# Performance work log

Hardware: AMD Instinct MI355X
Metric: run time of the kernel (lower is better)

Reference implementation:

```python
import jax, jax.numpy as jnp
import numpy as np

D_MODEL = 1024
D_STATE = 16
D_CONV = 4
EXPAND = 2
D_INNER = EXPAND * D_MODEL          # 2048
DT_RANK = D_MODEL // 16             # 64
BATCH, SEQ = 4, 2048


def setup_inputs() -> dict:
    key = jax.random.key(0)
    ks = jax.random.split(key, 8)
    s = lambda k, shape, sc=0.02: jax.random.normal(k, shape, jnp.float32) * sc
    x = jax.random.normal(ks[0], (BATCH, SEQ, D_MODEL), jnp.float32)
    tau = jax.random.uniform(ks[1], (BATCH, SEQ), jnp.float32) * 7200.0  # seconds
    # S4D-real init for A
    A_log = jnp.log(jnp.broadcast_to(jnp.arange(1, D_STATE + 1, dtype=jnp.float32), (D_INNER, D_STATE)))
    return dict(
        x=x, tau=tau,
        ln_g=jnp.ones((D_MODEL,), jnp.float32),
        ln_b=jnp.zeros((D_MODEL,), jnp.float32),
        in_proj_w=s(ks[2], (2 * D_INNER, D_MODEL)),
        conv_w=s(ks[3], (D_INNER, 1, D_CONV), 0.1),   # depthwise [O, I/g=1, K]
        conv_b=jnp.zeros((D_INNER,), jnp.float32),
        x_proj_w=s(ks[4], (DT_RANK + 2 * D_STATE, D_INNER)),
        dt_proj_w=s(ks[5], (D_INNER, DT_RANK), 0.1),
        dt_proj_b=jnp.full((D_INNER,), -4.6, jnp.float32),  # softplus ~ 0.01
        A_log=A_log,
        D=jnp.ones((D_INNER,), jnp.float32),
        out_proj_w=s(ks[6], (D_MODEL, D_INNER)),
        log_decay=jnp.full((D_MODEL,), -3.0, jnp.float32),
    )


def _mamba_block(x, tau, ln_g, ln_b, in_proj_w, conv_w, conv_b, x_proj_w,
                 dt_proj_w, dt_proj_b, A_log, D, out_proj_w, log_decay):
    # LayerNorm(d_model)
    mu = jnp.mean(x, axis=-1, keepdims=True)
    var = jnp.var(x, axis=-1, keepdims=True)
    xn = (x - mu) * jax.lax.rsqrt(var + 1e-5) * ln_g + ln_b

    # in_proj -> split into conv branch and gate branch, each [B, L, d_inner]
    xz = jnp.einsum('bld,ed->ble', xn, in_proj_w)
    x_in, z = jnp.split(xz, 2, axis=-1)

    # causal depthwise conv1d over time
    xc = jax.lax.conv_general_dilated(
        x_in.transpose(0, 2, 1), conv_w, (1,), [(D_CONV - 1, 0)],
        dimension_numbers=('NCH', 'OIH', 'NCH'), feature_group_count=D_INNER)
    u = jax.nn.silu(xc.transpose(0, 2, 1) + conv_b)          # [B, L, d_inner]

    # input-dependent SSM params
    x_dbl = jnp.einsum('ble,fe->blf', u, x_proj_w)
    dt, Bm, Cm = jnp.split(x_dbl, [DT_RANK, DT_RANK + D_STATE], axis=-1)
    delta = jax.nn.softplus(jnp.einsum('blr,dr->bld', dt, dt_proj_w) + dt_proj_b)
    A = -jnp.exp(A_log)                                       # [d_inner, d_state]

    # selective scan: h_t = exp(dt*A)*h + dt*u*B_t ; y_t = <h_t, C_t>
    def step(h, inp):
        d_t, B_t, C_t, u_t = inp                              # [B,d],[B,n],[B,n],[B,d]
        h = jnp.exp(d_t[..., None] * A) * h + (d_t * u_t)[..., None] * B_t[:, None, :]
        return h, jnp.einsum('bdn,bn->bd', h, C_t)

    h0 = jnp.zeros((x.shape[0], D_INNER, D_STATE), x.dtype)
    xs = (delta.transpose(1, 0, 2), Bm.transpose(1, 0, 2),
          Cm.transpose(1, 0, 2), u.transpose(1, 0, 2))
    _, ys = jax.lax.scan(step, h0, xs)
    y = ys.transpose(1, 0, 2) + u * D
    y = y * jax.nn.silu(z)
    h_out = jnp.einsum('ble,de->bld', y, out_proj_w)          # mamba output [B,L,d_model]

    # ZOH time-decay gate + residual (dropout = identity in eval)
    tau_h = jnp.maximum(tau / 3600.0, 1e-4)[..., None]
    gate = jnp.exp(-jax.nn.softplus(log_decay) * tau_h)
    return x + h_out * gate


def reference(x, tau, ln_g, ln_b, in_proj_w, conv_w, conv_b, x_proj_w,
              dt_proj_w, dt_proj_b, A_log, D, out_proj_w, log_decay):
    return _mamba_block(x, tau, ln_g, ln_b, in_proj_w, conv_w, conv_b, x_proj_w,
                        dt_proj_w, dt_proj_b, A_log, D, out_proj_w, log_decay)
```

## Files before the change

kernel.cpp:

```cpp
#include <hip/hip_runtime.h>

typedef unsigned short u16;
typedef unsigned int u32;
typedef short s16x8 __attribute__((ext_vector_type(8)));
typedef u16 u16x8 __attribute__((ext_vector_type(8)));
typedef float f32x4 __attribute__((ext_vector_type(4)));

#define TOK 8192
#define DM 1024
#define DI 2048
#define DS 16
#define DR 64
#define NCHUNK 64
#define CH 32
#define XPN 96
#define XP_SPLIT 4
#define CONV_T 16

#define SBAR() do { asm volatile("" ::: "memory"); __builtin_amdgcn_s_barrier(); asm volatile("" ::: "memory"); } while (0)
#define WAITVM(N) do { asm volatile("s_waitcnt vmcnt(" #N ")" ::: "memory"); __builtin_amdgcn_sched_barrier(0); } while (0)
#define WAITLGKM0() do { asm volatile("s_waitcnt lgkmcnt(0)" ::: "memory"); __builtin_amdgcn_sched_barrier(0); } while (0)

__device__ __forceinline__ u16 f2bf(float f) {
    u32 u = __float_as_uint(f);
    u32 r = (u + 0x7fffu + ((u >> 16) & 1u)) >> 16;
    return (u16)r;
}
__device__ __forceinline__ float bf2f(u16 h) {
    return __uint_as_float(((u32)h) << 16);
}
__device__ __forceinline__ float softplus_f(float x) {
    return (x > 15.f) ? x : __logf(1.f + __expf(x));
}
__device__ __forceinline__ void unpack8(const uint4 v, float* o) {
    o[0] = __uint_as_float(v.x << 16); o[1] = __uint_as_float(v.x & 0xffff0000u);
    o[2] = __uint_as_float(v.y << 16); o[3] = __uint_as_float(v.y & 0xffff0000u);
    o[4] = __uint_as_float(v.z << 16); o[5] = __uint_as_float(v.z & 0xffff0000u);
    o[6] = __uint_as_float(v.w << 16); o[7] = __uint_as_float(v.w & 0xffff0000u);
}
__device__ __forceinline__ void async16(u16* lds, const u16* g) {
    __builtin_amdgcn_global_load_lds(
        (const __attribute__((address_space(1))) void*)g,
        (__attribute__((address_space(3))) void*)lds, 16, 0, 0);
}

__global__ __launch_bounds__(256) void cvt_all(
    const float* __restrict__ in_w, const float* __restrict__ xp_w,
    const float* __restrict__ dt_w, const float* __restrict__ out_w,
    const float* __restrict__ tau, const float* __restrict__ log_decay,
    u16* __restrict__ wi, u16* __restrict__ wxp, u16* __restrict__ wdt,
    u16* __restrict__ wout, float* __restrict__ th, float* __restrict__ sd) {
    const int b = blockIdx.x;
    const float* src; u16* dst; int i;
    if (b < 4096)      { src = in_w;  dst = wi;   i = b * 256 + threadIdx.x; }
    else if (b < 4288) { src = xp_w;  dst = wxp;  i = (b - 4096) * 256 + threadIdx.x; }
    else if (b < 4416) { src = dt_w;  dst = wdt;  i = (b - 4288) * 256 + threadIdx.x; }
    else if (b < 6464) { src = out_w; dst = wout; i = (b - 4416) * 256 + threadIdx.x; }
    else {
        int j = (b - 6464) * 256 + threadIdx.x;
        if (j < TOK) th[j] = fmaxf(tau[j] * (1.f / 3600.f), 1e-4f);
        if (j < DM)  sd[j] = softplus_f(log_decay[j]);
        return;
    }
    float4 v = ((const float4*)src)[i];
    ushort4 o;
    o.x = f2bf(v.x); o.y = f2bf(v.y); o.z = f2bf(v.z); o.w = f2bf(v.w);
    ((ushort4*)dst)[i] = o;
}

__global__ __launch_bounds__(256) void ln_kernel(const float* __restrict__ x,
                                                 const float* __restrict__ g,
                                                 const float* __restrict__ bb,
                                                 u16* __restrict__ xn) {
    const int tok = blockIdx.x;
    const float4 v = ((const float4*)(x + (size_t)tok * DM))[threadIdx.x];
    float s = v.x + v.y + v.z + v.w;
    float sq = v.x * v.x + v.y * v.y + v.z * v.z + v.w * v.w;
#pragma unroll
    for (int off = 32; off; off >>= 1) {
        s += __shfl_xor(s, off);
        sq += __shfl_xor(sq, off);
    }
    __shared__ float red[8];
    const int wv = threadIdx.x >> 6;
    if ((threadIdx.x & 63) == 0) { red[wv] = s; red[4 + wv] = sq; }
    __syncthreads();
    s = red[0] + red[1] + red[2] + red[3];
    sq = red[4] + red[5] + red[6] + red[7];
    const float mean = s * (1.f / DM);
    const float var = sq * (1.f / DM) - mean * mean;
    const float rstd = rsqrtf(var + 1e-5f);
    const float4 gv = ((const float4*)g)[threadIdx.x];
    const float4 bv = ((const float4*)bb)[threadIdx.x];
    ushort4 o;
    o.x = f2bf((v.x - mean) * rstd * gv.x + bv.x);
    o.y = f2bf((v.y - mean) * rstd * gv.y + bv.y);
    o.z = f2bf((v.z - mean) * rstd * gv.z + bv.z);
    o.w = f2bf((v.w - mean) * rstd * gv.w + bv.w);
    ((ushort4*)(xn + (size_t)tok * DM))[threadIdx.x] = o;
}

template <int EPI>
__global__ __launch_bounds__(256, 2) void gemm128(
    const u16* __restrict__ A, int lda,
    const u16* __restrict__ W, int ldw, int K,
    u16* __restrict__ Cxi, u16* __restrict__ Cz,
    float* __restrict__ Cf,
    const float* __restrict__ xres, const float* __restrict__ th,
    const float* __restrict__ sd) {
    __shared__ __align__(16) u16 lds[2 * 16384];
    const int tid = threadIdx.x;
    const int wave = tid >> 6, lane = tid & 63;
    const int wm = wave >> 1, wn = wave & 1;
    const int fl = lane & 15, fh = lane >> 4;
    int bm, bn;
    if (EPI == 0) {
        const int swz = ((int)blockIdx.x & 7) * 256 + ((int)blockIdx.x >> 3);
        const int rg = swz >> 5, wi_ = swz & 31;
        bm = (rg >> 2) * 4 + (wi_ >> 3);
        bn = (rg & 3) * 8 + (wi_ & 7);
    } else {
        const int swz = ((int)blockIdx.x & 7) * 64 + ((int)blockIdx.x >> 3);
        const int rg = swz >> 4, wi_ = swz & 15;
        bm = (rg >> 1) * 4 + (wi_ >> 2);
        bn = (rg & 1) * 4 + (wi_ & 3);
    }
    const int NT = K >> 6;

    const int r0 = tid >> 3;
    const int cb = ((tid & 7) ^ (r0 & 7)) << 3;
    const int rA = bm * 128 + r0;
    const int rB = bn * 128 + r0;

    f32x4 acc[4][4];
#pragma unroll
    for (int m = 0; m < 4; m++)
#pragma unroll
        for (int n = 0; n < 4; n++) acc[m][n] = f32x4{0.f, 0.f, 0.f, 0.f};

    auto stage = [&](int buf, int k0) {
#pragma unroll
        for (int j = 0; j < 4; j++)
            async16(lds + buf * 16384 + j * 2048 + tid * 8,
                    A + (size_t)(rA + j * 32) * lda + k0 + cb);
#pragma unroll
        for (int j = 0; j < 4; j++)
            async16(lds + buf * 16384 + 8192 + j * 2048 + tid * 8,
                    W + (size_t)(rB + j * 32) * ldw + k0 + cb);
    };
    auto rdA = [&](int buf, int mf, int kk) -> s16x8 {
        int r = wm * 64 + mf * 16 + fl;
        int slot = ((kk << 2) | fh) ^ (fl & 7);
        return *(const s16x8*)(lds + buf * 16384 + r * 64 + slot * 8);
    };
    auto rdB = [&](int buf, int nf, int kk) -> s16x8 {
        int r = wn * 64 + nf * 16 + fl;
        int slot = ((kk << 2) | fh) ^ (fl & 7);
        return *(const s16x8*)(lds + buf * 16384 + 8192 + r * 64 + slot * 8);
    };

    stage(0, 0);
    stage(1, 64);
    WAITVM(8);
    SBAR();

    for (int t = 0; t < NT; ++t) {
        const int cur = t & 1;
        s16x8 ah[4][2], bh[4][2];
#pragma unroll
        for (int mf = 0; mf < 4; mf++) { ah[mf][0] = rdA(cur, mf, 0); ah[mf][1] = rdA(cur, mf, 1); }
#pragma unroll
        for (int nf = 0; nf < 4; nf++) { bh[nf][0] = rdB(cur, nf, 0); bh[nf][1] = rdB(cur, nf, 1); }
        WAITLGKM0();
        SBAR();
        if (t + 2 < NT) stage(cur, (t + 2) << 6);
        __builtin_amdgcn_s_setprio(1);
#pragma unroll
        for (int kk = 0; kk < 2; kk++)
#pragma unroll
            for (int mf = 0; mf < 4; mf++)
#pragma unroll
                for (int nf = 0; nf < 4; nf++)
                    acc[mf][nf] = __builtin_amdgcn_mfma_f32_16x16x32_bf16(ah[mf][kk], bh[nf][kk], acc[mf][nf], 0, 0, 0);
        __builtin_amdgcn_s_setprio(0);
        __builtin_amdgcn_sched_barrier(0);
        if (t + 2 < NT) { WAITVM(8); }
        else           { WAITVM(0); }
        SBAR();
    }

#pragma unroll
    for (int mf = 0; mf < 4; mf++)
#pragma unroll
        for (int j = 0; j < 4; j++) {
            int row = bm * 128 + wm * 64 + mf * 16 + fh * 4 + j;
            if (EPI == 0) {
                u16* dst = (bn < 16) ? Cxi : Cz;
                const int cbase = (bn < 16) ? bn * 128 : (bn - 16) * 128;
#pragma unroll
                for (int n = 0; n < 4; n++) {
                    int col = cbase + wn * 64 + n * 16 + fl;
                    dst[(size_t)row * DI + col] = f2bf(acc[mf][n][j]);
                }
            } else {
                float t = th[row];
#pragma unroll
                for (int n = 0; n < 4; n++) {
                    int col = bn * 128 + wn * 64 + n * 16 + fl;
                    size_t idx = (size_t)row * DM + col;
                    Cf[idx] = xres[idx] + acc[mf][n][j] * __expf(-sd[col] * t);
                }
            }
        }
}

__global__ __launch_bounds__(256) void gemm_bt(
    const u16* __restrict__ A, int lda,
    const u16* __restrict__ W,
    u16* __restrict__ Cb, int ldc,
    int M, int N, int K,
    const float* __restrict__ bias) {
    __shared__ u16 As[128 * 32];
    __shared__ u16 Bs[128 * 32];
    const int tid = threadIdx.x;
    const int wave = tid >> 6, lane = tid & 63;
    const int bm = blockIdx.x, bn = blockIdx.y;
    const int srow = lane >> 2, scol = (lane & 3) * 8;
    const int wr = wave >> 1, wc = wave & 1;
    const int fl = lane & 15, fh = lane >> 4;

    f32x4 acc[4][4];
#pragma unroll
    for (int m = 0; m < 4; m++)
#pragma unroll
        for (int n = 0; n < 4; n++) acc[m][n] = f32x4{0.f, 0.f, 0.f, 0.f};

    int ra[2], rb[2];
    u16* ldsA[2]; u16* ldsB[2];
#pragma unroll
    for (int i = 0; i < 2; i++) {
        int r = (wave * 2 + i) * 16 + srow;
        ra[i] = min(bm * 128 + r, M - 1);
        rb[i] = min(bn * 128 + r, N - 1);
        ldsA[i] = As + (wave * 2 + i) * 512 + lane * 8;
        ldsB[i] = Bs + (wave * 2 + i) * 512 + lane * 8;
    }

    for (int k0 = 0; k0 < K; k0 += 32) {
        __syncthreads();
#pragma unroll
        for (int i = 0; i < 2; i++) {
            async16(ldsA[i], A + (size_t)ra[i] * lda + k0 + scol);
            async16(ldsB[i], W + (size_t)rb[i] * K + k0 + scol);
        }
        __syncthreads();
        s16x8 av[4], bv[4];
#pragma unroll
        for (int m = 0; m < 4; m++)
            av[m] = *(const s16x8*)(As + (wr * 64 + m * 16 + fl) * 32 + fh * 8);
#pragma unroll
        for (int n = 0; n < 4; n++)
            bv[n] = *(const s16x8*)(Bs + (wc * 64 + n * 16 + fl) * 32 + fh * 8);
#pragma unroll
        for (int m = 0; m < 4; m++)
#pragma unroll
            for (int n = 0; n < 4; n++)
                acc[m][n] = __builtin_amdgcn_mfma_f32_16x16x32_bf16(av[m], bv[n], acc[m][n], 0, 0, 0);
    }

#pragma unroll
    for (int m = 0; m < 4; m++) {
#pragma unroll
        for (int j = 0; j < 4; j++) {
            int row = bm * 128 + wr * 64 + m * 16 + fh * 4 + j;
            if (row >= M) continue;
#pragma unroll
            for (int n = 0; n < 4; n++) {
                int col = bn * 128 + wc * 64 + n * 16 + fl;
                if (col >= N) continue;
                Cb[(size_t)row * ldc + col] = f2bf(softplus_f(acc[m][n][j] + bias[col]));
            }
        }
    }
}

__global__ __launch_bounds__(256) void xp_gemm(const u16* __restrict__ A,
                                               const u16* __restrict__ W,
                                               float* __restrict__ part) {
    __shared__ u16 As[128 * 64];
    __shared__ u16 Bs[XPN * 64];
    const int tid = threadIdx.x;
    const int wave = tid >> 6, lane = tid & 63;
    const int bm = blockIdx.x, sp = blockIdx.y;
    const int fl = lane & 15, fh = lane >> 4;
    const int trow = tid >> 3, tcol = (tid & 7) * 8;

    f32x4 acc[2][6];
#pragma unroll
    for (int m = 0; m < 2; m++)
#pragma unroll
        for (int n = 0; n < 6; n++) acc[m][n] = f32x4{0.f, 0.f, 0.f, 0.f};

    const int kbeg = sp * (DI / XP_SPLIT);
    for (int k0 = kbeg; k0 < kbeg + DI / XP_SPLIT; k0 += 64) {
        __syncthreads();
#pragma unroll
        for (int i = 0; i < 4; i++)
            async16(As + i * 2048 + tid * 8,
                    A + (size_t)(bm * 128 + i * 32 + trow) * DI + k0 + tcol);
#pragma unroll
        for (int i = 0; i < 3; i++)
            async16(Bs + i * 2048 + tid * 8,
                    W + (size_t)(i * 32 + trow) * DI + k0 + tcol);
        __syncthreads();
#pragma unroll
        for (int kk = 0; kk < 2; kk++) {
            s16x8 av[2], bv[6];
#pragma unroll
            for (int m = 0; m < 2; m++)
                av[m] = *(const s16x8*)(As + (wave * 32 + m * 16 + fl) * 64 + kk * 32 + fh * 8);
#pragma unroll
            for (int n = 0; n < 6; n++)
                bv[n] = *(const s16x8*)(Bs + (n * 16 + fl) * 64 + kk * 32 + fh * 8);
#pragma unroll
            for (int m = 0; m < 2; m++)
#pragma unroll
                for (int n = 0; n < 6; n++)
                    acc[m][n] = __builtin_amdgcn_mfma_f32_16x16x32_bf16(av[m], bv[n], acc[m][n], 0, 0, 0);
        }
    }
    float* dst = part + (size_t)sp * TOK * XPN;
#pragma unroll
    for (int m = 0; m < 2; m++)
#pragma unroll
        for (int j = 0; j < 4; j++) {
            int row = bm * 128 + wave * 32 + m * 16 + fh * 4 + j;
#pragma unroll
            for (int n = 0; n < 6; n++) {
                int col = n * 16 + fl;
                dst[(size_t)row * XPN + col] = acc[m][n][j];
            }
        }
}

__global__ __launch_bounds__(256) void xp_reduce(const float* __restrict__ part,
                                                 u16* __restrict__ out) {
    int i = blockIdx.x * 256 + threadIdx.x;
    if (i >= TOK * XPN) return;
    float s = 0.f;
#pragma unroll
    for (int sp = 0; sp < XP_SPLIT; sp++) s += part[(size_t)sp * TOK * XPN + i];
    out[i] = f2bf(s);
}

__global__ __launch_bounds__(256) void conv_silu_kernel(const u16* __restrict__ xi,
                                                        const float* __restrict__ cw,
                                                        const float* __restrict__ cb,
                                                        u16* __restrict__ u) {
    const int b = blockIdx.y;
    const int l0 = blockIdx.x * CONV_T;
    const int d0 = threadIdx.x * 8;
    float w0[8], w1[8], w2[8], w3[8], bias[8];
#pragma unroll
    for (int e = 0; e < 8; e++) {
        float4 wv = ((const float4*)cw)[d0 + e];
        w0[e] = wv.x; w1[e] = wv.y; w2[e] = wv.z; w3[e] = wv.w;
        bias[e] = cb[d0 + e];
    }
    float win[4][8];
#pragma unroll
    for (int i = 0; i < 3; i++) {
        int l = l0 - 3 + i;
        int slot = (l0 + 1 + i) & 3;
        if (l < 0) {
#pragma unroll
            for (int e = 0; e < 8; e++) win[slot][e] = 0.f;
        } else {
            u16x8 v = *(const u16x8*)(xi + ((size_t)(b * 2048 + l)) * DI + d0);
#pragma unroll
            for (int e = 0; e < 8; e++) win[slot][e] = bf2f(v[e]);
        }
    }
#pragma unroll
    for (int t = 0; t < CONV_T; t++) {
        const int l = l0 + t;
        const size_t tok = (size_t)b * 2048 + l;
        u16x8 v = *(const u16x8*)(xi + tok * DI + d0);
        const int s3 = t & 3;
#pragma unroll
        for (int e = 0; e < 8; e++) win[s3][e] = bf2f(v[e]);
        const int s0 = (t + 1) & 3, s1 = (t + 2) & 3, s2 = (t + 3) & 3;
        u16x8 o;
#pragma unroll
        for (int e = 0; e < 8; e++) {
            float a = bias[e];
            a = fmaf(w0[e], win[s0][e], a);
            a = fmaf(w1[e], win[s1][e], a);
            a = fmaf(w2[e], win[s2][e], a);
            a = fmaf(w3[e], win[s3][e], a);
            o[e] = f2bf(a / (1.f + __expf(-a)));
        }
        *(u16x8*)(u + tok * DI + d0) = o;
    }
}

__global__ __launch_bounds__(256) void scan_passA(const u16* __restrict__ delta,
                                                  const u16* __restrict__ u,
                                                  const u16* __restrict__ xdbl,
                                                  const float* __restrict__ A_log,
                                                  float* __restrict__ qh,
                                                  float* __restrict__ Sarr) {
    const int d = blockIdx.x * 256 + threadIdx.x;
    const int b = blockIdx.y, c = blockIdx.z;
    float Av[16];
#pragma unroll
    for (int n = 0; n < 16; n++) Av[n] = -__expf(A_log[d * 16 + n]);
    bool fast = true;
#pragma unroll
    for (int n = 0; n < 16; n++) fast = fast && (fabsf(Av[n] + (float)(n + 1)) < 1e-4f * (n + 1));
    const bool allfast = __all(fast);

    float h[16];
#pragma unroll
    for (int n = 0; n < 16; n++) h[n] = 0.f;
    float S = 0.f;
    const int l0 = c * CH;
    size_t tok = (size_t)b * 2048 + l0;
    float dt = bf2f(delta[tok * DI + d]);
    float uu = bf2f(u[tok * DI + d]);
    const uint4* bp0 = (const uint4*)(xdbl + tok * 96 + 64);
    uint4 b0 = bp0[0], b1 = bp0[1];
    for (int t = 0; t < CH; ++t) {
        const int tn = (t + 1 < CH) ? t + 1 : t;
        const size_t tokn = (size_t)b * 2048 + l0 + tn;
        float dt_n = bf2f(delta[tokn * DI + d]);
        float uu_n = bf2f(u[tokn * DI + d]);
        const uint4* bpn = (const uint4*)(xdbl + tokn * 96 + 64);
        uint4 b0n = bpn[0], b1n = bpn[1];
        float du = dt * uu;
        float Bv[16];
        unpack8(b0, Bv); unpack8(b1, Bv + 8);
        float e[16];
        if (allfast) {
            float r = __expf(-dt);
            e[0] = r;
#pragma unroll
            for (int n = 1; n < 16; n++) e[n] = e[n - 1] * r;
        } else {
#pragma unroll
            for (int n = 0; n < 16; n++) e[n] = __expf(dt * Av[n]);
        }
#pragma unroll
        for (int n = 0; n < 16; n++) h[n] = fmaf(e[n], h[n], du * Bv[n]);
        S += dt;
        dt = dt_n; uu = uu_n; b0 = b0n; b1 = b1n;
    }
    const size_t base = ((size_t)(c * 4 + b) * 16) * DI + d;
#pragma unroll
    for (int n = 0; n < 16; n++) qh[base + (size_t)n * DI] = h[n];
    Sarr[(size_t)(c * 4 + b) * DI + d] = S;
}

__global__ __launch_bounds__(256) void scan_passB(float* __restrict__ qh,
                                                  const float* __restrict__ Sarr,
                                                  const float* __restrict__ A_log) {
    const int idx = blockIdx.x * 256 + threadIdx.x;
    const int d = idx & (DI - 1);
    const int n = (idx >> 11) & 15;
    const int b = idx >> 15;
    const float Avn = -__expf(A_log[d * 16 + n]);
    float h = 0.f;
    for (int c = 0; c < NCHUNK; c++) {
        const size_t base = ((size_t)(c * 4 + b) * 16 + n) * DI + d;
        const float qv = qh[base];
        const float S = Sarr[(size_t)(c * 4 + b) * DI + d];
        qh[base] = h;
        h = fmaf(__expf(Avn * S), h, qv);
    }
}

__global__ __launch_bounds__(256) void scan_passC(const u16* __restrict__ delta,
                                                  const u16* __restrict__ u,
                                                  const u16* __restrict__ xdbl,
                                                  const u16* __restrict__ z,
                                                  const float* __restrict__ A_log,
                                                  const float* __restrict__ Dvec,
                                                  const float* __restrict__ qh,
                                                  u16* __restrict__ yg) {
    const int d = blockIdx.x * 256 + threadIdx.x;
    const int b = blockIdx.y, c = blockIdx.z;
    float Av[16];
#pragma unroll
    for (int n = 0; n < 16; n++) Av[n] = -__expf(A_log[d * 16 + n]);
    bool fast = true;
#pragma unroll
    for (int n = 0; n < 16; n++) fast = fast && (fabsf(Av[n] + (float)(n + 1)) < 1e-4f * (n + 1));
    const bool allfast = __all(fast);
    const float Dd = Dvec[d];

    float h[16];
    const size_t hbase = ((size_t)(c * 4 + b) * 16) * DI + d;
#pragma unroll
    for (int n = 0; n < 16; n++) h[n] = qh[hbase + (size_t)n * DI];

    const int l0 = c * CH;
    size_t tok = (size_t)b * 2048 + l0;
    float dt = bf2f(delta[tok * DI + d]);
    float uu = bf2f(u[tok * DI + d]);
    float zz = bf2f(z[tok * DI + d]);
    const uint4* bp0 = (const uint4*)(xdbl + tok * 96 + 64);
    uint4 b0 = bp0[0], b1 = bp0[1], c0 = bp0[2], c1 = bp0[3];
    for (int t = 0; t < CH; ++t) {
        const int tn = (t + 1 < CH) ? t + 1 : t;
        const size_t tokn = (size_t)b * 2048 + l0 + tn;
        float dt_n = bf2f(delta[tokn * DI + d]);
        float uu_n = bf2f(u[tokn * DI + d]);
        float zz_n = bf2f(z[tokn * DI + d]);
        const uint4* bpn = (const uint4*)(xdbl + tokn * 96 + 64);
        uint4 b0n = bpn[0], b1n = bpn[1], c0n = bpn[2], c1n = bpn[3];

        float du = dt * uu;
        float Bv[16], Cv[16];
        unpack8(b0, Bv); unpack8(b1, Bv + 8);
        unpack8(c0, Cv); unpack8(c1, Cv + 8);
        float e[16];
        if (allfast) {
            float r = __expf(-dt);
            e[0] = r;
#pragma unroll
            for (int n = 1; n < 16; n++) e[n] = e[n - 1] * r;
        } else {
#pragma unroll
            for (int n = 0; n < 16; n++) e[n] = __expf(dt * Av[n]);
        }
        float y = 0.f;
#pragma unroll
        for (int n = 0; n < 16; n++) {
            h[n] = fmaf(e[n], h[n], du * Bv[n]);
            y = fmaf(h[n], Cv[n], y);
        }
        float sz = zz / (1.f + __expf(-zz));
        const size_t tokc = (size_t)b * 2048 + l0 + t;
        yg[tokc * DI + d] = f2bf((y + uu * Dd) * sz);

        dt = dt_n; uu = uu_n; zz = zz_n;
        b0 = b0n; b1 = b1n; c0 = c0n; c1 = c1n;
    }
}

extern "C" void kernel_launch(void* const* d_in, const int* in_sizes, int n_in,
                              void* d_out, int out_size, void* d_ws, size_t ws_size,
                              hipStream_t stream) {
    const float* x = (const float*)d_in[0];
    const float* tau = (const float*)d_in[1];
    const float* ln_g = (const float*)d_in[2];
    const float* ln_b = (const float*)d_in[3];
    const float* in_proj_w = (const float*)d_in[4];
    const float* conv_w = (const float*)d_in[5];
    const float* conv_b = (const float*)d_in[6];
    const float* x_proj_w = (const float*)d_in[7];
    const float* dt_proj_w = (const float*)d_in[8];
    const float* dt_proj_b = (const float*)d_in[9];
    const float* A_log = (const float*)d_in[10];
    const float* Dvec = (const float*)d_in[11];
    const float* out_proj_w = (const float*)d_in[12];
    const float* log_decay = (const float*)d_in[13];
    float* out = (float*)d_out;

    char* ws = (char*)d_ws;
    size_t off = 0;
    auto alloc = [&](size_t bytes) -> void* {
        void* p = ws + off;
        off += (bytes + 255) & ~(size_t)255;
        return p;
    };
    u16* xn    = (u16*)alloc((size_t)TOK * DM * 2);
    u16* w_in  = (u16*)alloc((size_t)2 * DI * DM * 2);
    u16* w_xp  = (u16*)alloc((size_t)XPN * DI * 2);
    u16* w_dt  = (u16*)alloc((size_t)DI * DR * 2);
    u16* w_out = (u16*)alloc((size_t)DM * DI * 2);
    u16* xi    = (u16*)alloc((size_t)TOK * DI * 2);
    u16* z     = (u16*)alloc((size_t)TOK * DI * 2);
    u16* u     = (u16*)alloc((size_t)TOK * DI * 2);
    u16* xdbl  = (u16*)alloc((size_t)TOK * XPN * 2);
    u16* delta = (u16*)alloc((size_t)TOK * DI * 2);
    float* qh   = (float*)alloc((size_t)NCHUNK * 4 * 16 * DI * 4);
    float* Sarr = (float*)alloc((size_t)NCHUNK * 4 * DI * 4);
    u16* yg    = (u16*)alloc((size_t)TOK * DI * 2);
    float* th = (float*)alloc((size_t)TOK * 4);
    float* sd = (float*)alloc((size_t)DM * 4);
    float* xp_part = (float*)xn;

    cvt_all<<<6496, 256, 0, stream>>>(in_proj_w, x_proj_w, dt_proj_w, out_proj_w,
                                      tau, log_decay, w_in, w_xp, w_dt, w_out, th, sd);

    ln_kernel<<<TOK, 256, 0, stream>>>(x, ln_g, ln_b, xn);

    gemm128<0><<<2048, 256, 0, stream>>>(xn, DM, w_in, DM, DM, xi, z,
                                         nullptr, nullptr, nullptr, nullptr);
    conv_silu_kernel<<<dim3(2048 / CONV_T, 4), 256, 0, stream>>>(xi, conv_w, conv_b, u);

    xp_gemm<<<dim3(64, XP_SPLIT), 256, 0, stream>>>(u, w_xp, xp_part);
    xp_reduce<<<(TOK * XPN + 255) / 256, 256, 0, stream>>>(xp_part, xdbl);

    gemm_bt<<<dim3(64, 16), 256, 0, stream>>>(xdbl, XPN, w_dt, delta, DI,
                                              TOK, DI, DR, dt_proj_b);

    scan_passA<<<dim3(8, 4, NCHUNK), 256, 0, stream>>>(delta, u, xdbl, A_log, qh, Sarr);
    scan_passB<<<512, 256, 0, stream>>>(qh, Sarr, A_log);
    scan_passC<<<dim3(8, 4, NCHUNK), 256, 0, stream>>>(delta, u, xdbl, z, A_log, Dvec, qh, yg);

    gemm128<2><<<512, 256, 0, stream>>>(yg, DI, w_out, DI, DI, nullptr, nullptr,
                                        out, x, th, sd);
}
```

Before: 307.5 us.

## Merge layernorm into prep kernel, specialize dt GEMM, store chunk states in bf16

Folds the LayerNorm launch into the weight-conversion kernel so both run as a single launch with extra blocks. Replaces the generic K-looped dt-projection GEMM with one specialized for K=64: all of A and W is loaded once into XOR-swizzled LDS, with no bounds checks. Stores the inter-chunk scan states qh as bf16 instead of fp32, halving their traffic across the three scan passes. The bf16 state storage reduces precision of carried hidden states, which could affect accuracy.

```diff
diff --git a/kernel.cpp b/kernel.cpp
--- a/kernel.cpp
+++ b/kernel.cpp
@@ -44,13 +44,45 @@
         (__attribute__((address_space(3))) void*)lds, 16, 0, 0);
 }
 
-__global__ __launch_bounds__(256) void cvt_all(
+__global__ __launch_bounds__(256) void prep_all(
     const float* __restrict__ in_w, const float* __restrict__ xp_w,
     const float* __restrict__ dt_w, const float* __restrict__ out_w,
     const float* __restrict__ tau, const float* __restrict__ log_decay,
+    const float* __restrict__ x, const float* __restrict__ ln_g,
+    const float* __restrict__ ln_b,
     u16* __restrict__ wi, u16* __restrict__ wxp, u16* __restrict__ wdt,
-    u16* __restrict__ wout, float* __restrict__ th, float* __restrict__ sd) {
+    u16* __restrict__ wout, float* __restrict__ th, float* __restrict__ sd,
+    u16* __restrict__ xn) {
     const int b = blockIdx.x;
+    if (b >= 6496) {
+        const int tok = b - 6496;
+        const float4 v = ((const float4*)(x + (size_t)tok * DM))[threadIdx.x];
+        float s = v.x + v.y + v.z + v.w;
+        float sq = v.x * v.x + v.y * v.y + v.z * v.z + v.w * v.w;
+#pragma unroll
+        for (int off = 32; off; off >>= 1) {
+            s += __shfl_xor(s, off);
+            sq += __shfl_xor(sq, off);
+        }
+        __shared__ float red[8];
+        const int wv = threadIdx.x >> 6;
+        if ((threadIdx.x & 63) == 0) { red[wv] = s; red[4 + wv] = sq; }
+        __syncthreads();
+        s = red[0] + red[1] + red[2] + red[3];
+        sq = red[4] + red[5] + red[6] + red[7];
+        const float mean = s * (1.f / DM);
+        const float var = sq * (1.f / DM) - mean * mean;
+        const float rstd = rsqrtf(var + 1e-5f);
+        const float4 gv = ((const float4*)ln_g)[threadIdx.x];
+        const float4 bv = ((const float4*)ln_b)[threadIdx.x];
+        ushort4 o;
+        o.x = f2bf((v.x - mean) * rstd * gv.x + bv.x);
+        o.y = f2bf((v.y - mean) * rstd * gv.y + bv.y);
+        o.z = f2bf((v.z - mean) * rstd * gv.z + bv.z);
+        o.w = f2bf((v.w - mean) * rstd * gv.w + bv.w);
+        ((ushort4*)(xn + (size_t)tok * DM))[threadIdx.x] = o;
+        return;
+    }
     const float* src; u16* dst; int i;
     if (b < 4096)      { src = in_w;  dst = wi;   i = b * 256 + threadIdx.x; }
     else if (b < 4288) { src = xp_w;  dst = wxp;  i = (b - 4096) * 256 + threadIdx.x; }
@@ -66,38 +98,6 @@
     ushort4 o;
     o.x = f2bf(v.x); o.y = f2bf(v.y); o.z = f2bf(v.z); o.w = f2bf(v.w);
     ((ushort4*)dst)[i] = o;
-}
-
-__global__ __launch_bounds__(256) void ln_kernel(const float* __restrict__ x,
-                                                 const float* __restrict__ g,
-                                                 const float* __restrict__ bb,
-                                                 u16* __restrict__ xn) {
-    const int tok = blockIdx.x;
-    const float4 v = ((const float4*)(x + (size_t)tok * DM))[threadIdx.x];
-    float s = v.x + v.y + v.z + v.w;
-    float sq = v.x * v.x + v.y * v.y + v.z * v.z + v.w * v.w;
-#pragma unroll
-    for (int off = 32; off; off >>= 1) {
-        s += __shfl_xor(s, off);
-        sq += __shfl_xor(sq, off);
-    }
-    __shared__ float red[8];
-    const int wv = threadIdx.x >> 6;
-    if ((threadIdx.x & 63) == 0) { red[wv] = s; red[4 + wv] = sq; }
-    __syncthreads();
-    s = red[0] + red[1] + red[2] + red[3];
-    sq = red[4] + red[5] + red[6] + red[7];
-    const float mean = s * (1.f / DM);
-    const float var = sq * (1.f / DM) - mean * mean;
-    const float rstd = rsqrtf(var + 1e-5f);
-    const float4 gv = ((const float4*)g)[threadIdx.x];
-    const float4 bv = ((const float4*)bb)[threadIdx.x];
-    ushort4 o;
-    o.x = f2bf((v.x - mean) * rstd * gv.x + bv.x);
-    o.y = f2bf((v.y - mean) * rstd * gv.y + bv.y);
-    o.z = f2bf((v.z - mean) * rstd * gv.z + bv.z);
-    o.w = f2bf((v.w - mean) * rstd * gv.w + bv.w);
-    ((ushort4*)(xn + (size_t)tok * DM))[threadIdx.x] = o;
 }
 
 template <int EPI>
@@ -214,20 +214,42 @@
         }
 }
 
-__global__ __launch_bounds__(256) void gemm_bt(
-    const u16* __restrict__ A, int lda,
+__global__ __launch_bounds__(256) void dt_gemm(
+    const u16* __restrict__ A,
     const u16* __restrict__ W,
-    u16* __restrict__ Cb, int ldc,
-    int M, int N, int K,
+    u16* __restrict__ Cb,
     const float* __restrict__ bias) {
-    __shared__ u16 As[128 * 32];
-    __shared__ u16 Bs[128 * 32];
+    __shared__ __align__(16) u16 lds[2 * 8192];
     const int tid = threadIdx.x;
     const int wave = tid >> 6, lane = tid & 63;
+    const int wm = wave >> 1, wn = wave & 1;
+    const int fl = lane & 15, fh = lane >> 4;
     const int bm = blockIdx.x, bn = blockIdx.y;
-    const int srow = lane >> 2, scol = (lane & 3) * 8;
-    const int wr = wave >> 1, wc = wave & 1;
-    const int fl = lane & 15, fh = lane >> 4;
+
+    const int r0 = tid >> 3;
+    const int cb = ((tid & 7) ^ (r0 & 7)) << 3;
+
+#pragma unroll
+    for (int j = 0; j < 4; j++)
+        async16(lds + j * 2048 + tid * 8,
+                A + (size_t)(bm * 128 + j * 32 + r0) * XPN + cb);
+#pragma unroll
+    for (int j = 0; j < 4; j++)
+        async16(lds + 8192 + j * 2048 + tid * 8,
+                W + (size_t)(bn * 128 + j * 32 + r0) * DR + cb);
+    WAITVM(0);
+    SBAR();
+
+    auto rdA = [&](int mf, int kk) -> s16x8 {
+        int r = wm * 64 + mf * 16 + fl;
+        int slot = ((kk << 2) | fh) ^ (fl & 7);
+        return *(const s16x8*)(lds + r * 64 + slot * 8);
+    };
+    auto rdB = [&](int nf, int kk) -> s16x8 {
+        int r = wn * 64 + nf * 16 + fl;
+        int slot = ((kk << 2) | fh) ^ (fl & 7);
+        return *(const s16x8*)(lds + 8192 + r * 64 + slot * 8);
+    };
 
     f32x4 acc[4][4];
 #pragma unroll
@@ -235,53 +257,31 @@
 #pragma unroll
         for (int n = 0; n < 4; n++) acc[m][n] = f32x4{0.f, 0.f, 0.f, 0.f};
 
-    int ra[2], rb[2];
-    u16* ldsA[2]; u16* ldsB[2];
-#pragma unroll
-    for (int i = 0; i < 2; i++) {
-        int r = (wave * 2 + i) * 16 + srow;
-        ra[i] = min(bm * 128 + r, M - 1);
-        rb[i] = min(bn * 128 + r, N - 1);
-        ldsA[i] = As + (wave * 2 + i) * 512 + lane * 8;
-        ldsB[i] = Bs + (wave * 2 + i) * 512 + lane * 8;
-    }
-
-    for (int k0 = 0; k0 < K; k0 += 32) {
-        __syncthreads();
-#pragma unroll
-        for (int i = 0; i < 2; i++) {
-            async16(ldsA[i], A + (size_t)ra[i] * lda + k0 + scol);
-            async16(ldsB[i], W + (size_t)rb[i] * K + k0 + scol);
-        }
-        __syncthreads();
-        s16x8 av[4], bv[4];
-#pragma unroll
-        for (int m = 0; m < 4; m++)
-            av[m] = *(const s16x8*)(As + (wr * 64 + m * 16 + fl) * 32 + fh * 8);
-#pragma unroll
-        for (int n = 0; n < 4; n++)
-            bv[n] = *(const s16x8*)(Bs + (wc * 64 + n * 16 + fl) * 32 + fh * 8);
-#pragma unroll
-        for (int m = 0; m < 4; m++)
-#pragma unroll
-            for (int n = 0; n < 4; n++)
-                acc[m][n] = __builtin_amdgcn_mfma_f32_16x16x32_bf16(av[m], bv[n], acc[m][n], 0, 0, 0);
-    }
-
-#pragma unroll
-    for (int m = 0; m < 4; m++) {
+    s16x8 ah[4][2], bh[4][2];
+#pragma unroll
+    for (int mf = 0; mf < 4; mf++) { ah[mf][0] = rdA(mf, 0); ah[mf][1] = rdA(mf, 1); }
+#pragma unroll
+    for (int nf = 0; nf < 4; nf++) { bh[nf][0] = rdB(nf, 0); bh[nf][1] = rdB(nf, 1); }
+    WAITLGKM0();
+#pragma unroll
+    for (int kk = 0; kk < 2; kk++)
+#pragma unroll
+        for (int mf = 0; mf < 4; mf++)
+#pragma unroll
+            for (int nf = 0; nf < 4; nf++)
+                acc[mf][nf] = __builtin_amdgcn_mfma_f32_16x16x32_bf16(ah[mf][kk], bh[nf][kk], acc[mf][nf], 0, 0, 0);
+
+#pragma unroll
+    for (int mf = 0; mf < 4; mf++)
 #pragma unroll
         for (int j = 0; j < 4; j++) {
-            int row = bm * 128 + wr * 64 + m * 16 + fh * 4 + j;
-            if (row >= M) continue;
+            int row = bm * 128 + wm * 64 + mf * 16 + fh * 4 + j;
 #pragma unroll
             for (int n = 0; n < 4; n++) {
-                int col = bn * 128 + wc * 64 + n * 16 + fl;
-                if (col >= N) continue;
-                Cb[(size_t)row * ldc + col] = f2bf(softplus_f(acc[m][n][j] + bias[col]));
+                int col = bn * 128 + wn * 64 + n * 16 + fl;
+                Cb[(size_t)row * DI + col] = f2bf(softplus_f(acc[mf][n][j] + bias[col]));
             }
         }
-    }
 }
 
 __global__ __launch_bounds__(256) void xp_gemm(const u16* __restrict__ A,
@@ -408,7 +408,7 @@
                                                   const u16* __restrict__ u,
                                                   const u16* __restrict__ xdbl,
                                                   const float* __restrict__ A_log,
-                                                  float* __restrict__ qh,
+                                                  u16* __restrict__ qh,
                                                   float* __restrict__ Sarr) {
     const int d = blockIdx.x * 256 + threadIdx.x;
     const int b = blockIdx.y, c = blockIdx.z;
@@ -457,11 +457,11 @@
     }
     const size_t base = ((size_t)(c * 4 + b) * 16) * DI + d;
 #pragma unroll
-    for (int n = 0; n < 16; n++) qh[base + (size_t)n * DI] = h[n];
+    for (int n = 0; n < 16; n++) qh[base + (size_t)n * DI] = f2bf(h[n]);
     Sarr[(size_t)(c * 4 + b) * DI + d] = S;
 }
 
-__global__ __launch_bounds__(256) void scan_passB(float* __restrict__ qh,
+__global__ __launch_bounds__(256) void scan_passB(u16* __restrict__ qh,
                                                   const float* __restrict__ Sarr,
                                                   const float* __restrict__ A_log) {
     const int idx = blockIdx.x * 256 + threadIdx.x;
@@ -472,9 +472,9 @@
     float h = 0.f;
     for (int c = 0; c < NCHUNK; c++) {
         const size_t base = ((size_t)(c * 4 + b) * 16 + n) * DI + d;
-        const float qv = qh[base];
+        const float qv = bf2f(qh[base]);
         const float S = Sarr[(size_t)(c * 4 + b) * DI + d];
-        qh[base] = h;
+        qh[base] = f2bf(h);
         h = fmaf(__expf(Avn * S), h, qv);
     }
 }
@@ -485,7 +485,7 @@
                                                   const u16* __restrict__ z,
                                                   const float* __restrict__ A_log,
                                                   const float* __restrict__ Dvec,
-                                                  const float* __restrict__ qh,
+                                                  const u16* __restrict__ qh,
                                                   u16* __restrict__ yg) {
     const int d = blockIdx.x * 256 + threadIdx.x;
     const int b = blockIdx.y, c = blockIdx.z;
@@ -501,7 +501,7 @@
     float h[16];
     const size_t hbase = ((size_t)(c * 4 + b) * 16) * DI + d;
 #pragma unroll
-    for (int n = 0; n < 16; n++) h[n] = qh[hbase + (size_t)n * DI];
+    for (int n = 0; n < 16; n++) h[n] = bf2f(qh[hbase + (size_t)n * DI]);
 
     const int l0 = c * CH;
     size_t tok = (size_t)b * 2048 + l0;
@@ -584,17 +584,16 @@
     u16* u     = (u16*)alloc((size_t)TOK * DI * 2);
     u16* xdbl  = (u16*)alloc((size_t)TOK * XPN * 2);
     u16* delta = (u16*)alloc((size_t)TOK * DI * 2);
-    float* qh   = (float*)alloc((size_t)NCHUNK * 4 * 16 * DI * 4);
+    u16* qh    = (u16*)alloc((size_t)NCHUNK * 4 * 16 * DI * 2);
     float* Sarr = (float*)alloc((size_t)NCHUNK * 4 * DI * 4);
     u16* yg    = (u16*)alloc((size_t)TOK * DI * 2);
     float* th = (float*)alloc((size_t)TOK * 4);
     float* sd = (float*)alloc((size_t)DM * 4);
     float* xp_part = (float*)xn;
 
-    cvt_all<<<6496, 256, 0, stream>>>(in_proj_w, x_proj_w, dt_proj_w, out_proj_w,
-                                      tau, log_decay, w_in, w_xp, w_dt, w_out, th, sd);
-
-    ln_kernel<<<TOK, 256, 0, stream>>>(x, ln_g, ln_b, xn);
+    prep_all<<<6496 + TOK, 256, 0, stream>>>(in_proj_w, x_proj_w, dt_proj_w, out_proj_w,
+                                             tau, log_decay, x, ln_g, ln_b,
+                                             w_in, w_xp, w_dt, w_out, th, sd, xn);
 
     gemm128<0><<<2048, 256, 0, stream>>>(xn, DM, w_in, DM, DM, xi, z,
                                          nullptr, nullptr, nullptr, nullptr);
@@ -603,8 +602,7 @@
     xp_gemm<<<dim3(64, XP_SPLIT), 256, 0, stream>>>(u, w_xp, xp_part);
     xp_reduce<<<(TOK * XPN + 255) / 256, 256, 0, stream>>>(xp_part, xdbl);
 
-    gemm_bt<<<dim3(64, 16), 256, 0, stream>>>(xdbl, XPN, w_dt, delta, DI,
-                                              TOK, DI, DR, dt_proj_b);
+    dt_gemm<<<dim3(64, 16), 256, 0, stream>>>(xdbl, w_dt, delta, dt_proj_b);
 
     scan_passA<<<dim3(8, 4, NCHUNK), 256, 0, stream>>>(delta, u, xdbl, A_log, qh, Sarr);
     scan_passB<<<512, 256, 0, stream>>>(qh, Sarr, A_log);
```

Result: faster. 281.5 us, median of 2 (-8.4%).
